# Performance work log

Measured on AMD Instinct MI355X. Metric: run time of the kernel, lower is better.

Reference implementation:

```python
import jax, jax.numpy as jnp
import numpy as np
from jax import lax

B, C, P = 8, 32, 256      # batch, channels, patch side
KB = 2                    # buf_region = kernel_size - stride = 3 - 1
R_MASK = 1                # output_bypassing: last-column patch, r = small_padding = 1


def setup_inputs() -> dict:
    key = jax.random.key(0)
    ks = jax.random.split(key, 5)
    x = jax.random.normal(ks[0], (B, C, P, P), jnp.float32)
    # right-halo stored by the left-neighbor patch (store_right -> last 2 cols)
    rbuf = jax.random.normal(ks[1], (B, C, P, KB), jnp.float32)
    # bottom-halo stored by the top-neighbor patch AFTER its hcat (width P+2)
    bbuf = jax.random.normal(ks[2], (B, C, KB, P + KB), jnp.float32)
    W = jax.random.normal(ks[3], (C, C, 3, 3), jnp.float32) * 0.05
    bias = jax.random.normal(ks[4], (C,), jnp.float32) * 0.05
    return {"x": x, "rbuf": rbuf, "bbuf": bbuf, "W": W, "bias": bias}


def reference(x, rbuf, bbuf, W, bias):
    # output_bypassing: zero the rightmost R_MASK columns (image right edge)
    x = x.at[:, :, :, -R_MASK:].set(0.0)
    # hcat: prepend right-halo from left neighbor -> [B,C,P,P+2]
    x = jnp.concatenate([rbuf, x], axis=-1)
    # vcat: prepend bottom-halo from top neighbor -> [B,C,P+2,P+2]
    x = jnp.concatenate([bbuf, x], axis=-2)
    # (store_bot side effect omitted: pure function returns conv output only)
    out = lax.conv_general_dilated(
        x, W, window_strides=(1, 1), padding='VALID',
        dimension_numbers=('NCHW', 'OIHW', 'NCHW'))  # -> [B,C,P,P]
    return out + bias[None, :, None, None]
```

## Files before the change

kernel.cpp:

```cpp
#include <hip/hip_runtime.h>
#include <cstdint>


constexpr int B  = 8;
constexpr int C  = 32;
constexpr int P  = 256;
constexpr int KB = 2;
constexpr int TS = 16;
constexpr int RS = 18;
constexpr int PL = 324;
constexpr int XSZ = 16 * PL;
constexpr int LDSZ = 9856;

typedef short bf16x8 __attribute__((ext_vector_type(8)));
typedef float f32x4  __attribute__((ext_vector_type(4)));
union Frag { uint32_t u[4]; bf16x8 v; };

static __device__ __forceinline__ uint32_t pk_bf16(float lo, float hi) {
    uint32_t a  = __builtin_bit_cast(uint32_t, lo);
    uint32_t b2 = __builtin_bit_cast(uint32_t, hi);
    a  += 0x7FFFu + ((a  >> 16) & 1u);
    b2 += 0x7FFFu + ((b2 >> 16) & 1u);
    return (a >> 16) | (b2 & 0xFFFF0000u);
}

__global__ __launch_bounds__(256) void pack_w_kernel(
    const float* __restrict__ W, uint32_t* __restrict__ wpk)
{
    const int g = blockIdx.x * 256 + threadIdx.x;
    const float4 v = ((const float4*)W)[g];
    const float vv[4] = { v.x, v.y, v.z, v.w };
    uint16_t* wh = (uint16_t*)wpk;
    #pragma unroll
    for (int e = 0; e < 4; ++e) {
        const int flat = 4 * g + e;
        const int t    = flat % 9;
        const int rest = flat / 9;
        const int ic   = rest & 31;
        const int oc   = rest >> 5;
        const uint32_t u = __builtin_bit_cast(uint32_t, vv[e]);
        const uint16_t h = (uint16_t)((u + 0x7FFFu + ((u >> 16) & 1u)) >> 16);
        wh[(t * 512 + oc * 16 + (ic >> 1)) * 2 + (ic & 1)] = h;
    }
}

struct St16 {
    float4 a0, c0;
    float  h0l, h0h, h1l, h1h;
};

__global__ __launch_bounds__(256, 2) void conv_mfma(
    const float* __restrict__ x,
    const float* __restrict__ rbuf,
    const float* __restrict__ bbuf,
    const uint32_t* __restrict__ wpk,
    const float* __restrict__ bias,
    float* __restrict__ out)
{
    const int tid  = threadIdx.x;
    const int lane = tid & 63;
    const int w    = tid >> 6;
    const int q    = lane >> 4;
    const int n16  = lane & 15;

    const int sw = (blockIdx.x & 7) * 256 + (blockIdx.x >> 3);
    const int b  = sw >> 8;
    const int ty = (sw >> 4) & 15;
    const int cx = sw & 15;
    const int x0 = cx * TS, y0 = ty * TS;

    __shared__ uint32_t Xs[LDSZ];

    const int srow = lane >> 2;
    const int scol = (lane & 3) * 4;
    const bool zc  = (cx == 15) && ((lane & 3) == 3);

    int h_ldso[2], h_ps[2];
    const float* h_bp[2];
    bool h_z[2];
    {
        const float* xb0 = x    + (size_t)b * C * P * P;
        const float* rb0 = rbuf + (size_t)b * C * P * KB;
        const float* bb0 = bbuf + (size_t)b * C * KB * (P + KB);
        const float* basep[3] = { xb0, rb0, bb0 };
        const int    psz[3]   = { P * P, P * KB, KB * (P + KB) };
        #pragma unroll
        for (int ci = 0; ci < 2; ++ci) {
            const int c = lane + 64 * ci;
            int prow, pcol;
            if (c < 36) { const int hr = (c >= 18) ? 1 : 0; prow = hr; pcol = c - 18 * hr; }
            else        { const int cc = c - 36; prow = KB + (cc >> 1); pcol = cc & 1; }
            h_ldso[ci] = prow * RS + pcol;
            const int gr = y0 + prow, gc = x0 + pcol;
            int sel, off; bool z = false;
            if (gr < KB)      { sel = 2; off = gr * (P + KB) + gc; }
            else if (gc < KB) { sel = 1; off = (gr - KB) * KB + gc; }
            else              { sel = 0; off = (gr - KB) * P + (gc - KB);
                                z = (gc == P + KB - 1); }
            h_bp[ci] = basep[sel] + off;
            h_ps[ci] = psz[sel];
            h_z[ci]  = z;
        }
    }
    const bool h1a = lane < 4;

    const float* xb = x + (size_t)b * C * P * P;

    St16 S[4];
    #pragma unroll
    for (int k2 = 0; k2 < 4; ++k2) {
        const int m = 4 * k2 + w;
        const float* pi = xb + (size_t)(2 * m) * (P * P) + (y0 + srow) * P + x0 + scol;
        S[k2].a0 = *(const float4*)pi;
        S[k2].c0 = *(const float4*)(pi + P * P);
        const float* p0 = h_bp[0] + (size_t)(2 * m) * h_ps[0];
        S[k2].h0l = h_z[0] ? 0.f : p0[0];
        S[k2].h0h = h_z[0] ? 0.f : p0[h_ps[0]];
        if (h1a) {
            const float* p1 = h_bp[1] + (size_t)(2 * m) * h_ps[1];
            S[k2].h1l = h_z[1] ? 0.f : p1[0];
            S[k2].h1h = h_z[1] ? 0.f : p1[h_ps[1]];
        }
    }

    #pragma unroll
    for (int k2 = 0; k2 < 4; ++k2) {
        const int m = 4 * k2 + w;
        float4 a0 = S[k2].a0, c0 = S[k2].c0;
        if (zc) { a0.w = 0.f; c0.w = 0.f; }
        uint2 p0, p1;
        p0.x = pk_bf16(a0.x, c0.x); p0.y = pk_bf16(a0.y, c0.y);
        p1.x = pk_bf16(a0.z, c0.z); p1.y = pk_bf16(a0.w, c0.w);
        uint32_t* base = Xs + m * PL + (srow + KB) * RS + KB + scol;
        *(uint2*)(base + 0) = p0;
        *(uint2*)(base + 2) = p1;
        Xs[m * PL + h_ldso[0]] = pk_bf16(S[k2].h0l, S[k2].h0h);
        if (h1a) Xs[m * PL + h_ldso[1]] = pk_bf16(S[k2].h1l, S[k2].h1h);
    }

    Frag Bf[9][2];
    #pragma unroll
    for (int t = 0; t < 9; ++t)
        #pragma unroll
        for (int oh = 0; oh < 2; ++oh)
            *(uint4*)Bf[t][oh].u =
                *(const uint4*)&wpk[t * 512 + (oh * 16 + n16) * 16 + q * 4];
    #pragma unroll
    for (int t = 0; t < 9; ++t)
        #pragma unroll
        for (int oh = 0; oh < 2; ++oh)
            #pragma unroll
            for (int p = 0; p < 4; ++p)
                asm volatile("" : "+v"(Bf[t][oh].u[p]));
    const float bv0 = bias[n16];
    const float bv1 = bias[16 + n16];

    __syncthreads();

    f32x4 acc[4][2];
    #pragma unroll
    for (int rr = 0; rr < 4; ++rr)
        #pragma unroll
        for (int oh = 0; oh < 2; ++oh)
            #pragma unroll
            for (int e = 0; e < 4; ++e) acc[rr][oh][e] = 0.f;

    #pragma unroll
    for (int dr = 0; dr < 6; ++dr) {
        Frag A[3];
        const uint32_t* ap = Xs + (4 * q) * PL + (4 * w + dr) * RS + n16;
        #pragma unroll
        for (int kx = 0; kx < 3; ++kx)
            #pragma unroll
            for (int p = 0; p < 4; ++p)
                A[kx].u[p] = ap[p * PL + kx];
        #pragma unroll
        for (int ky = 0; ky < 3; ++ky) {
            const int rr = dr - ky;
            if (rr >= 0 && rr < 4) {
                #pragma unroll
                for (int kx = 0; kx < 3; ++kx) {
                    acc[rr][0] = __builtin_amdgcn_mfma_f32_16x16x32_bf16(
                                     A[kx].v, Bf[ky * 3 + kx][0].v, acc[rr][0], 0, 0, 0);
                    acc[rr][1] = __builtin_amdgcn_mfma_f32_16x16x32_bf16(
                                     A[kx].v, Bf[ky * 3 + kx][1].v, acc[rr][1], 0, 0, 0);
                }
            }
        }
    }

    #pragma unroll
    for (int oh = 0; oh < 2; ++oh) {
        const int oc = oh * 16 + n16;
        const float bv = oh ? bv1 : bv0;
        #pragma unroll
        for (int rr = 0; rr < 4; ++rr) {
            float4 v;
            v.x = acc[rr][oh][0] + bv;
            v.y = acc[rr][oh][1] + bv;
            v.z = acc[rr][oh][2] + bv;
            v.w = acc[rr][oh][3] + bv;
            *(float4*)&out[((size_t)(b * C + oc) * P + (y0 + 4 * w + rr)) * P
                           + x0 + 4 * q] = v;
        }
    }
}

extern "C" void kernel_launch(void* const* d_in, const int* in_sizes, int n_in,
                              void* d_out, int out_size, void* d_ws, size_t ws_size,
                              hipStream_t stream) {
    const float* x    = (const float*)d_in[0];
    const float* rbuf = (const float*)d_in[1];
    const float* bbuf = (const float*)d_in[2];
    const float* W    = (const float*)d_in[3];
    const float* bias = (const float*)d_in[4];
    float* out = (float*)d_out;
    uint32_t* wpk = (uint32_t*)d_ws;

    pack_w_kernel<<<9, 256, 0, stream>>>(W, wpk);
    conv_mfma<<<2048, 256, 0, stream>>>(x, rbuf, bbuf, wpk, bias, out);
}
```

Measured before the change: 137.7 us.

## Process two row tiles per block with prefetch and LDS-staged weights

Each block now handles two vertically adjacent 16x16 tiles, halving the grid. The global loads for the next tile are issued in the middle of the current tile's MFMA loop so their latency overlaps compute. Weights are pre-packed in fragment order and staged once into LDS per block, then read from LDS into registers for each tile, instead of every block issuing scattered global loads. This trades extra LDS use, two extra barriers per tile and fewer blocks (less parallelism) for better latency hiding and amortized setup.

```diff
diff --git a/kernel.cpp b/kernel.cpp
--- a/kernel.cpp
+++ b/kernel.cpp
@@ -10,7 +10,8 @@
 constexpr int RS = 18;
 constexpr int PL = 324;
 constexpr int XSZ = 16 * PL;
-constexpr int LDSZ = 9856;
+constexpr int WOFF = XSZ;
+constexpr int LDSZ = XSZ + 4608;
 
 typedef short bf16x8 __attribute__((ext_vector_type(8)));
 typedef float f32x4  __attribute__((ext_vector_type(4)));
@@ -27,21 +28,17 @@
 __global__ __launch_bounds__(256) void pack_w_kernel(
     const float* __restrict__ W, uint32_t* __restrict__ wpk)
 {
-    const int g = blockIdx.x * 256 + threadIdx.x;
-    const float4 v = ((const float4*)W)[g];
-    const float vv[4] = { v.x, v.y, v.z, v.w };
-    uint16_t* wh = (uint16_t*)wpk;
-    #pragma unroll
-    for (int e = 0; e < 4; ++e) {
-        const int flat = 4 * g + e;
-        const int t    = flat % 9;
-        const int rest = flat / 9;
-        const int ic   = rest & 31;
-        const int oc   = rest >> 5;
-        const uint32_t u = __builtin_bit_cast(uint32_t, vv[e]);
-        const uint16_t h = (uint16_t)((u + 0x7FFFu + ((u >> 16) & 1u)) >> 16);
-        wh[(t * 512 + oc * 16 + (ic >> 1)) * 2 + (ic & 1)] = h;
-    }
+    const int idx = blockIdx.x * 256 + threadIdx.x;
+    const int t   = idx >> 9;
+    const int r   = idx & 511;
+    const int oh  = r >> 8;
+    const int l   = (r >> 2) & 63;
+    const int p   = r & 3;
+    const int oc  = oh * 16 + (l & 15);
+    const int icp = 4 * (l >> 4) + p;
+    const float lo = W[(oc * C + 2 * icp) * 9 + t];
+    const float hi = W[(oc * C + 2 * icp + 1) * 9 + t];
+    wpk[idx] = pk_bf16(lo, hi);
 }
 
 struct St16 {
@@ -63,11 +60,11 @@
     const int q    = lane >> 4;
     const int n16  = lane & 15;
 
-    const int sw = (blockIdx.x & 7) * 256 + (blockIdx.x >> 3);
-    const int b  = sw >> 8;
-    const int ty = (sw >> 4) & 15;
-    const int cx = sw & 15;
-    const int x0 = cx * TS, y0 = ty * TS;
+    const int sw  = (blockIdx.x & 7) * 128 + (blockIdx.x >> 3);
+    const int b   = sw >> 7;
+    const int cx  = (sw >> 3) & 15;
+    const int typ = sw & 7;
+    const int x0  = cx * TS;
 
     __shared__ uint32_t Xs[LDSZ];
 
@@ -75,58 +72,58 @@
     const int scol = (lane & 3) * 4;
     const bool zc  = (cx == 15) && ((lane & 3) == 3);
 
-    int h_ldso[2], h_ps[2];
-    const float* h_bp[2];
-    bool h_z[2];
-    {
-        const float* xb0 = x    + (size_t)b * C * P * P;
-        const float* rb0 = rbuf + (size_t)b * C * P * KB;
-        const float* bb0 = bbuf + (size_t)b * C * KB * (P + KB);
-        const float* basep[3] = { xb0, rb0, bb0 };
-        const int    psz[3]   = { P * P, P * KB, KB * (P + KB) };
+    int prowA[2], pcolA[2], h_ldso[2];
+    #pragma unroll
+    for (int ci = 0; ci < 2; ++ci) {
+        const int c = lane + 64 * ci;
+        int prow, pcol;
+        if (c < 36) { const int hr = (c >= 18) ? 1 : 0; prow = hr; pcol = c - 18 * hr; }
+        else        { const int cc = c - 36; prow = KB + (cc >> 1); pcol = cc & 1; }
+        prowA[ci] = prow; pcolA[ci] = pcol;
+        h_ldso[ci] = prow * RS + pcol;
+    }
+    const bool h1a = lane < 4;
+
+    const float* xb = x    + (size_t)b * C * P * P;
+    const float* rb = rbuf + (size_t)b * C * P * KB;
+    const float* bb = bbuf + (size_t)b * C * KB * (P + KB);
+    const float* basep[3] = { xb, rb, bb };
+    const int    psz[3]   = { P * P, P * KB, KB * (P + KB) };
+
+    const float* h_bp[2]; int h_ps[2]; bool h_z[2];
+    auto mkh = [&](int y0) {
         #pragma unroll
         for (int ci = 0; ci < 2; ++ci) {
-            const int c = lane + 64 * ci;
-            int prow, pcol;
-            if (c < 36) { const int hr = (c >= 18) ? 1 : 0; prow = hr; pcol = c - 18 * hr; }
-            else        { const int cc = c - 36; prow = KB + (cc >> 1); pcol = cc & 1; }
-            h_ldso[ci] = prow * RS + pcol;
-            const int gr = y0 + prow, gc = x0 + pcol;
-            int sel, off; bool z = false;
+            const int gr = y0 + prowA[ci], gc = x0 + pcolA[ci];
+            int sel, off; bool zz = false;
             if (gr < KB)      { sel = 2; off = gr * (P + KB) + gc; }
             else if (gc < KB) { sel = 1; off = (gr - KB) * KB + gc; }
             else              { sel = 0; off = (gr - KB) * P + (gc - KB);
-                                z = (gc == P + KB - 1); }
+                                zz = (gc == P + KB - 1); }
             h_bp[ci] = basep[sel] + off;
             h_ps[ci] = psz[sel];
-            h_z[ci]  = z;
-        }
-    }
-    const bool h1a = lane < 4;
-
-    const float* xb = x + (size_t)b * C * P * P;
-
-    St16 S[4];
-    #pragma unroll
-    for (int k2 = 0; k2 < 4; ++k2) {
+            h_z[ci]  = zz;
+        }
+    };
+
+    auto ldk = [&](int k2, int y0, St16& S) {
         const int m = 4 * k2 + w;
         const float* pi = xb + (size_t)(2 * m) * (P * P) + (y0 + srow) * P + x0 + scol;
-        S[k2].a0 = *(const float4*)pi;
-        S[k2].c0 = *(const float4*)(pi + P * P);
+        S.a0 = *(const float4*)pi;
+        S.c0 = *(const float4*)(pi + P * P);
         const float* p0 = h_bp[0] + (size_t)(2 * m) * h_ps[0];
-        S[k2].h0l = h_z[0] ? 0.f : p0[0];
-        S[k2].h0h = h_z[0] ? 0.f : p0[h_ps[0]];
+        S.h0l = h_z[0] ? 0.f : p0[0];
+        S.h0h = h_z[0] ? 0.f : p0[h_ps[0]];
         if (h1a) {
             const float* p1 = h_bp[1] + (size_t)(2 * m) * h_ps[1];
-            S[k2].h1l = h_z[1] ? 0.f : p1[0];
-            S[k2].h1h = h_z[1] ? 0.f : p1[h_ps[1]];
-        }
-    }
-
-    #pragma unroll
-    for (int k2 = 0; k2 < 4; ++k2) {
+            S.h1l = h_z[1] ? 0.f : p1[0];
+            S.h1h = h_z[1] ? 0.f : p1[h_ps[1]];
+        }
+    };
+
+    auto stk = [&](int k2, const St16& S) {
         const int m = 4 * k2 + w;
-        float4 a0 = S[k2].a0, c0 = S[k2].c0;
+        float4 a0 = S.a0, c0 = S.c0;
         if (zc) { a0.w = 0.f; c0.w = 0.f; }
         uint2 p0, p1;
         p0.x = pk_bf16(a0.x, c0.x); p0.y = pk_bf16(a0.y, c0.y);
@@ -134,75 +131,139 @@
         uint32_t* base = Xs + m * PL + (srow + KB) * RS + KB + scol;
         *(uint2*)(base + 0) = p0;
         *(uint2*)(base + 2) = p1;
-        Xs[m * PL + h_ldso[0]] = pk_bf16(S[k2].h0l, S[k2].h0h);
-        if (h1a) Xs[m * PL + h_ldso[1]] = pk_bf16(S[k2].h1l, S[k2].h1h);
-    }
-
-    Frag Bf[9][2];
+        Xs[m * PL + h_ldso[0]] = pk_bf16(S.h0l, S.h0h);
+        if (h1a) Xs[m * PL + h_ldso[1]] = pk_bf16(S.h1l, S.h1h);
+    };
+
+    const uint4* wp4 = (const uint4*)wpk;
+    uint4 wv0 = wp4[tid];
+    uint4 wv1 = wp4[256 + tid];
+    uint4 wv2 = wp4[512 + tid];
+    uint4 wv3 = wp4[768 + tid];
+    uint4 wvt;
+    const bool wtail = tid < 128;
+    if (wtail) wvt = wp4[1024 + tid];
+
+    St16 Sn[4];
+    mkh(2 * typ * TS);
     #pragma unroll
-    for (int t = 0; t < 9; ++t)
-        #pragma unroll
-        for (int oh = 0; oh < 2; ++oh)
-            *(uint4*)Bf[t][oh].u =
-                *(const uint4*)&wpk[t * 512 + (oh * 16 + n16) * 16 + q * 4];
+    for (int k2 = 0; k2 < 4; ++k2) ldk(k2, 2 * typ * TS, Sn[k2]);
+
+    uint4* xsW = (uint4*)(Xs + WOFF);
+    xsW[tid]       = wv0;
+    xsW[256 + tid] = wv1;
+    xsW[512 + tid] = wv2;
+    xsW[768 + tid] = wv3;
+    if (wtail) xsW[1024 + tid] = wvt;
+
     #pragma unroll
-    for (int t = 0; t < 9; ++t)
-        #pragma unroll
-        for (int oh = 0; oh < 2; ++oh)
-            #pragma unroll
-            for (int p = 0; p < 4; ++p)
-                asm volatile("" : "+v"(Bf[t][oh].u[p]));
+    for (int k2 = 0; k2 < 4; ++k2) stk(k2, Sn[k2]);
+
     const float bv0 = bias[n16];
     const float bv1 = bias[16 + n16];
-
     __syncthreads();
 
-    f32x4 acc[4][2];
-    #pragma unroll
-    for (int rr = 0; rr < 4; ++rr)
-        #pragma unroll
-        for (int oh = 0; oh < 2; ++oh)
-            #pragma unroll
-            for (int e = 0; e < 4; ++e) acc[rr][oh][e] = 0.f;
-
-    #pragma unroll
-    for (int dr = 0; dr < 6; ++dr) {
-        Frag A[3];
-        const uint32_t* ap = Xs + (4 * q) * PL + (4 * w + dr) * RS + n16;
-        #pragma unroll
-        for (int kx = 0; kx < 3; ++kx)
-            #pragma unroll
-            for (int p = 0; p < 4; ++p)
-                A[kx].u[p] = ap[p * PL + kx];
-        #pragma unroll
-        for (int ky = 0; ky < 3; ++ky) {
-            const int rr = dr - ky;
-            if (rr >= 0 && rr < 4) {
+    #pragma unroll 1
+    for (int t = 0; t < 2; ++t) {
+        const int y0 = (2 * typ + t) * TS;
+
+        if (t < 1) {
+            mkh(y0 + TS);
+            ldk(0, y0 + TS, Sn[0]);
+            ldk(1, y0 + TS, Sn[1]);
+        }
+
+        Frag Bf[9][2];
+        #pragma unroll
+        for (int tt = 0; tt < 9; ++tt)
+            #pragma unroll
+            for (int oh = 0; oh < 2; ++oh)
+                *(uint4*)Bf[tt][oh].u =
+                    *(const uint4*)&Xs[WOFF + tt * 512 + oh * 256 + lane * 4];
+
+        f32x4 acc[4][2];
+        #pragma unroll
+        for (int rr = 0; rr < 4; ++rr)
+            #pragma unroll
+            for (int oh = 0; oh < 2; ++oh)
                 #pragma unroll
-                for (int kx = 0; kx < 3; ++kx) {
-                    acc[rr][0] = __builtin_amdgcn_mfma_f32_16x16x32_bf16(
-                                     A[kx].v, Bf[ky * 3 + kx][0].v, acc[rr][0], 0, 0, 0);
-                    acc[rr][1] = __builtin_amdgcn_mfma_f32_16x16x32_bf16(
-                                     A[kx].v, Bf[ky * 3 + kx][1].v, acc[rr][1], 0, 0, 0);
+                for (int e = 0; e < 4; ++e) acc[rr][oh][e] = 0.f;
+
+        #pragma unroll
+        for (int dr = 0; dr < 3; ++dr) {
+            Frag A[3];
+            const uint32_t* ap = Xs + (4 * q) * PL + (4 * w + dr) * RS + n16;
+            #pragma unroll
+            for (int kx = 0; kx < 3; ++kx)
+                #pragma unroll
+                for (int p = 0; p < 4; ++p)
+                    A[kx].u[p] = ap[p * PL + kx];
+            #pragma unroll
+            for (int ky = 0; ky < 3; ++ky) {
+                const int rr = dr - ky;
+                if (rr >= 0 && rr < 4) {
+                    #pragma unroll
+                    for (int kx = 0; kx < 3; ++kx) {
+                        acc[rr][0] = __builtin_amdgcn_mfma_f32_16x16x32_bf16(
+                                         A[kx].v, Bf[ky * 3 + kx][0].v, acc[rr][0], 0, 0, 0);
+                        acc[rr][1] = __builtin_amdgcn_mfma_f32_16x16x32_bf16(
+                                         A[kx].v, Bf[ky * 3 + kx][1].v, acc[rr][1], 0, 0, 0);
+                    }
                 }
             }
         }
-    }
-
-    #pragma unroll
-    for (int oh = 0; oh < 2; ++oh) {
-        const int oc = oh * 16 + n16;
-        const float bv = oh ? bv1 : bv0;
-        #pragma unroll
-        for (int rr = 0; rr < 4; ++rr) {
-            float4 v;
-            v.x = acc[rr][oh][0] + bv;
-            v.y = acc[rr][oh][1] + bv;
-            v.z = acc[rr][oh][2] + bv;
-            v.w = acc[rr][oh][3] + bv;
-            *(float4*)&out[((size_t)(b * C + oc) * P + (y0 + 4 * w + rr)) * P
-                           + x0 + 4 * q] = v;
-        }
+
+        if (t < 1) {
+            ldk(2, y0 + TS, Sn[2]);
+            ldk(3, y0 + TS, Sn[3]);
+        }
+
+        #pragma unroll
+        for (int dr = 3; dr < 6; ++dr) {
+            Frag A[3];
+            const uint32_t* ap = Xs + (4 * q) * PL + (4 * w + dr) * RS + n16;
+            #pragma unroll
+            for (int kx = 0; kx < 3; ++kx)
+                #pragma unroll
+                for (int p = 0; p < 4; ++p)
+                    A[kx].u[p] = ap[p * PL + kx];
+            #pragma unroll
+            for (int ky = 0; ky < 3; ++ky) {
+                const int rr = dr - ky;
+                if (rr >= 0 && rr < 4) {
+                    #pragma unroll
+                    for (int kx = 0; kx < 3; ++kx) {
+                        acc[rr][0] = __builtin_amdgcn_mfma_f32_16x16x32_bf16(
+                                         A[kx].v, Bf[ky * 3 + kx][0].v, acc[rr][0], 0, 0, 0);
+                        acc[rr][1] = __builtin_amdgcn_mfma_f32_16x16x32_bf16(
+                                         A[kx].v, Bf[ky * 3 + kx][1].v, acc[rr][1], 0, 0, 0);
+                    }
+                }
+            }
+        }
+
+        #pragma unroll
+        for (int oh = 0; oh < 2; ++oh) {
+            const int oc = oh * 16 + n16;
+            const float bv = oh ? bv1 : bv0;
+            #pragma unroll
+            for (int rr = 0; rr < 4; ++rr) {
+                float4 v;
+                v.x = acc[rr][oh][0] + bv;
+                v.y = acc[rr][oh][1] + bv;
+                v.z = acc[rr][oh][2] + bv;
+                v.w = acc[rr][oh][3] + bv;
+                *(float4*)&out[((size_t)(b * C + oc) * P + (y0 + 4 * w + rr)) * P
+                               + x0 + 4 * q] = v;
+            }
+        }
+
+        __syncthreads();
+        if (t < 1) {
+            #pragma unroll
+            for (int k2 = 0; k2 < 4; ++k2) stk(k2, Sn[k2]);
+        }
+        __syncthreads();
     }
 }
 
@@ -217,6 +278,6 @@
     float* out = (float*)d_out;
     uint32_t* wpk = (uint32_t*)d_ws;
 
-    pack_w_kernel<<<9, 256, 0, stream>>>(W, wpk);
-    conv_mfma<<<2048, 256, 0, stream>>>(x, rbuf, bbuf, wpk, bias, out);
-}
+    pack_w_kernel<<<18, 256, 0, stream>>>(W, wpk);
+    conv_mfma<<<1024, 256, 0, stream>>>(x, rbuf, bbuf, wpk, bias, out);
+}
```

Result: slower. 141.6 us (+2.9%).
